# Kernel optimization log

Measured on AMD Instinct MI355X. Metric: run time of the kernel, lower is better.

## Reference

```python
import jax, jax.numpy as jnp
import numpy as np

DIM = 768
H = 12
D = DIM // H            # 64
SCALE = D ** -0.5
M = 64                  # landmarks for pnp heads
PINV_ITERS = 6
PNP_HEADS = 11          # heads 0..10 use Nystrom, head 11 uses softmax


def setup_inputs() -> dict:
    key = jax.random.key(0)
    ks = jax.random.split(key, 5)
    B, N = 4, 4096
    x = jax.random.normal(ks[0], (B, N, DIM), jnp.float32)
    qkv_w = jax.random.normal(ks[1], (3 * DIM, DIM), jnp.float32) * (DIM ** -0.5)
    qkv_b = jax.random.normal(ks[2], (3 * DIM,), jnp.float32) * 0.01
    proj_w = jax.random.normal(ks[3], (DIM, DIM), jnp.float32) * (DIM ** -0.5)
    proj_b = jax.random.normal(ks[4], (DIM,), jnp.float32) * 0.01
    return {"x": x, "qkv_w": qkv_w, "qkv_b": qkv_b, "proj_w": proj_w, "proj_b": proj_b}


def moore_penrose_iter_pinv(x, iters=PINV_ITERS):
    # x: [B, h, M, M]. Original torch code takes torch.max over the whole per-head
    # tensor (incl. batch), so normalize with a per-head scalar over axes (B, M).
    abs_x = jnp.abs(x)
    col_max = abs_x.sum(axis=-1, keepdims=True).max(axis=(0, 2, 3), keepdims=True)
    row_max = abs_x.sum(axis=-2, keepdims=True).max(axis=(0, 2, 3), keepdims=True)
    z = jnp.swapaxes(x, -1, -2) / (col_max * row_max)
    I = jnp.eye(x.shape[-1], dtype=x.dtype)
    for _ in range(iters):
        xz = x @ z
        z = 0.25 * (z @ (13.0 * I - xz @ (15.0 * I - xz @ (7.0 * I - xz))))
    return z


def reference(x, qkv_w, qkv_b, proj_w, proj_b):
    B, N, C = x.shape
    qkv = (x @ qkv_w.T + qkv_b).reshape(B, N, 3, H, D).transpose(2, 0, 3, 1, 4)  # [3,B,H,N,D]
    q, k, v = qkv[0] * SCALE, qkv[1], qkv[2]

    # ---- Nystrom (pnp) heads 0..PNP_HEADS-1, all with the same M -> vectorized ----
    qp, kp, vp = q[:, :PNP_HEADS], k[:, :PNP_HEADS], v[:, :PNP_HEADS]
    idxs = jnp.array([int(i * N / M) for i in range(M)], dtype=jnp.int32)
    q_m = qp[:, :, idxs, :]   # [B,h,M,D] landmark queries
    k_m = kp[:, :, idxs, :]   # [B,h,M,D] landmark keys

    SA = jnp.einsum('bhnd,bhmd->bhnm', qp, k_m)   # [B,h,N,M]
    SC = jnp.einsum('bhmd,bhnd->bhmn', q_m, kp)   # [B,h,M,N]
    SB = jnp.einsum('bhmd,bhld->bhml', q_m, k_m)  # [B,h,M,M]

    eA = jnp.exp(SA - SA.max(axis=-1, keepdims=True))
    sc_max = SC.max(axis=-1, keepdims=True)       # [B,h,M,1]
    eC = jnp.exp(SC - sc_max)
    eB = jnp.exp(jnp.clip(SB - sc_max, -88.0, None))

    v_aug = jnp.concatenate([vp, jnp.ones_like(vp[..., :1])], axis=-1)  # [B,h,N,D+1]
    pi = moore_penrose_iter_pinv(eB)
    prod = (eA @ pi) @ (eC @ v_aug)               # [B,h,N,D+1]
    out_p = prod[..., :-1] / jnp.maximum(prod[..., -1:], 1e-8)

    # ---- fallback softmax head(s) ----
    qs, ks_, vs = q[:, PNP_HEADS:], k[:, PNP_HEADS:], v[:, PNP_HEADS:]
    attn = jax.nn.softmax(jnp.einsum('bhnd,bhmd->bhnm', qs, ks_), axis=-1)
    out_s = attn @ vs

    ctx = jnp.concatenate([out_p, out_s], axis=1).transpose(0, 2, 1, 3).reshape(B, N, C)
    return ctx @ proj_w.T + proj_b
```

## Files before the change

kernel.cpp:

```cpp
#include <hip/hip_runtime.h>


typedef __attribute__((ext_vector_type(8))) short short8;
typedef __attribute__((ext_vector_type(4))) float f32x4;
typedef __attribute__((ext_vector_type(4))) unsigned short ushort4v;

static __device__ __forceinline__ unsigned short f2bf(float f) {
    union { float f; unsigned u; } x; x.f = f;
    unsigned r = x.u + 0x7fffu + ((x.u >> 16) & 1u);
    return (unsigned short)(r >> 16);
}

static __device__ __forceinline__ void bfsplit(float x, unsigned short& h, unsigned short& l) {
    unsigned short hh = f2bf(x);
    union { unsigned u; float f; } t; t.u = (unsigned)hh << 16;
    h = hh;
    l = f2bf(x - t.f);
}

__global__ __launch_bounds__(256) void preconv(
    const float* __restrict__ in, unsigned short* __restrict__ hi,
    unsigned short* __restrict__ lo, int n4)
{
    for (int i = blockIdx.x * 256 + threadIdx.x; i < n4; i += gridDim.x * 256) {
        float4 f = *(const float4*)(in + (size_t)i * 4);
        float vs[4] = {f.x, f.y, f.z, f.w};
        ushort4v h, l;
        #pragma unroll
        for (int j = 0; j < 4; ++j) {
            unsigned short hh, ll;
            bfsplit(vs[j], hh, ll);
            h[j] = hh; l[j] = ll;
        }
        *(ushort4v*)(hi + (size_t)i * 4) = h;
        *(ushort4v*)(lo + (size_t)i * 4) = l;
    }
}

__global__ __launch_bounds__(256, 2) void gemm_qkv_mfma(
    const unsigned short* __restrict__ Xh, const unsigned short* __restrict__ Xl,
    const unsigned short* __restrict__ Wh, const unsigned short* __restrict__ Wl,
    const float* __restrict__ bias,
    float* __restrict__ q, float* __restrict__ k, float* __restrict__ v)
{
    __shared__ unsigned short Ah[4096], Al[4096], Bh[4096], Bl[4096];
    const int tid = threadIdx.x;
    const int bid = blockIdx.x;
    const int swz = (bid & 7) * 288 + (bid >> 3);
    const int brow = (swz / 18) << 7, bcol = (swz % 18) << 7;
    const int ln = tid & 63, wv = tid >> 6;
    const int wr = (wv >> 1) << 6, wc = (wv & 1) << 6;
    const int srow = tid >> 1, sc = (tid & 1) << 1;
    const size_t ag = (size_t)(brow + srow) * 768 + (sc << 3);
    const size_t bg = (size_t)(bcol + srow) * 768 + (sc << 3);
    const int fr = ln & 15, fc = ln >> 4;
    const int i0 = srow * 32 + (((sc + 0) ^ (srow & 3)) << 3);
    const int i1 = srow * 32 + (((sc + 1) ^ (srow & 3)) << 3);

    f32x4 acc[4][4] = {};
    for (int k0 = 0; k0 < 768; k0 += 32) {
        short8 xh0 = *(const short8*)(Xh + ag + k0);
        short8 xh1 = *(const short8*)(Xh + ag + k0 + 8);
        short8 xl0 = *(const short8*)(Xl + ag + k0);
        short8 xl1 = *(const short8*)(Xl + ag + k0 + 8);
        short8 wh0 = *(const short8*)(Wh + bg + k0);
        short8 wh1 = *(const short8*)(Wh + bg + k0 + 8);
        short8 wl0 = *(const short8*)(Wl + bg + k0);
        short8 wl1 = *(const short8*)(Wl + bg + k0 + 8);
        __syncthreads();
        *(short8*)&Ah[i0] = xh0; *(short8*)&Ah[i1] = xh1;
        *(short8*)&Al[i0] = xl0; *(short8*)&Al[i1] = xl1;
        *(short8*)&Bh[i0] = wh0; *(short8*)&Bh[i1] = wh1;
        *(short8*)&Bl[i0] = wl0; *(short8*)&Bl[i1] = wl1;
        __syncthreads();
        short8 ah[4], al[4], bh[4], bl[4];
        #pragma unroll
        for (int i = 0; i < 4; ++i) {
            int ar = wr + (i << 4) + fr;
            int aidx = ar * 32 + ((fc ^ (ar & 3)) << 3);
            ah[i] = *(short8*)&Ah[aidx];
            al[i] = *(short8*)&Al[aidx];
            int br2 = wc + (i << 4) + fr;
            int bidx = br2 * 32 + ((fc ^ (br2 & 3)) << 3);
            bh[i] = *(short8*)&Bh[bidx];
            bl[i] = *(short8*)&Bl[bidx];
        }
        #pragma unroll
        for (int i = 0; i < 4; ++i)
            #pragma unroll
            for (int j = 0; j < 4; ++j) {
                acc[i][j] = __builtin_amdgcn_mfma_f32_16x16x32_bf16(ah[i], bh[j], acc[i][j], 0, 0, 0);
                acc[i][j] = __builtin_amdgcn_mfma_f32_16x16x32_bf16(ah[i], bl[j], acc[i][j], 0, 0, 0);
                acc[i][j] = __builtin_amdgcn_mfma_f32_16x16x32_bf16(al[i], bh[j], acc[i][j], 0, 0, 0);
            }
    }
    const int fg = ln >> 4;
    #pragma unroll
    for (int j = 0; j < 4; ++j) {
        int c = bcol + wc + (j << 4) + fr;
        float bb = bias[c];
        int t = c / 768;
        int rem = c - t * 768;
        int h = rem >> 6, d = rem & 63;
        #pragma unroll
        for (int i = 0; i < 4; ++i)
            #pragma unroll
            for (int r = 0; r < 4; ++r) {
                int row = brow + wr + (i << 4) + (fg << 2) + r;
                int b = row >> 12, n = row & 4095;
                float val = acc[i][j][r] + bb;
                size_t idx = (((size_t)(b * 12 + h) << 12) + n) * 64 + d;
                if (t == 0)      q[idx] = val * 0.125f;
                else if (t == 1) k[idx] = val;
                else             v[idx] = val;
            }
    }
}

__global__ __launch_bounds__(256) void wflash(
    const float* __restrict__ q, const float* __restrict__ k,
    const float* __restrict__ v,
    float* __restrict__ wacc, float* __restrict__ wl, float* __restrict__ wm)
{
    int chunk = blockIdx.x;
    int bh = blockIdx.y;
    int b = bh / 11, h = bh - b * 11;
    size_t base = ((size_t)(b * 12 + h)) << 12;
    const float* qb = q + base * 64;
    const float* kb = k + base * 64;
    const float* vb = v + base * 64;
    __shared__ unsigned short kh[64][72], kl[64][72];
    __shared__ unsigned short vth[64][72], vtl[64][72];
    __shared__ unsigned short ph[4][16][72], pl[4][16][72];
    int tid = threadIdx.x;
    int wv = tid >> 6, ln = tid & 63;
    int rr = tid >> 2, dg = (tid & 3) << 4;
    const int arow = (wv << 4) + (ln & 15);
    const int ak0 = (ln >> 4) << 3;
    const int rg = (ln >> 4) << 2;
    short8 aqh0, aql0, aqh1, aql1;
    {
        const float* qrow = qb + ((size_t)arow << 12);
        #pragma unroll
        for (int j = 0; j < 8; ++j) {
            unsigned short hh, ll;
            bfsplit(qrow[ak0 + j], hh, ll);
            aqh0[j] = (short)hh; aql0[j] = (short)ll;
            bfsplit(qrow[ak0 + 32 + j], hh, ll);
            aqh1[j] = (short)hh; aql1[j] = (short)ll;
        }
    }
    f32x4 o_acc[4] = {};
    float mr[4] = {-1e30f, -1e30f, -1e30f, -1e30f};
    float lr[4] = {};
    for (int t = 0; t < 8; ++t) {
        int n0 = (chunk << 9) + (t << 6);
        __syncthreads();
        {
            const float* krow = kb + (((size_t)(n0 + rr)) << 6) + dg;
            const float* vrow = vb + (((size_t)(n0 + rr)) << 6) + dg;
            #pragma unroll
            for (int i = 0; i < 16; i += 4) {
                float4 f = *(const float4*)(krow + i);
                unsigned short hh, ll;
                bfsplit(f.x, hh, ll); kh[rr][dg+i]   = hh; kl[rr][dg+i]   = ll;
                bfsplit(f.y, hh, ll); kh[rr][dg+i+1] = hh; kl[rr][dg+i+1] = ll;
                bfsplit(f.z, hh, ll); kh[rr][dg+i+2] = hh; kl[rr][dg+i+2] = ll;
                bfsplit(f.w, hh, ll); kh[rr][dg+i+3] = hh; kl[rr][dg+i+3] = ll;
                float4 g2 = *(const float4*)(vrow + i);
                bfsplit(g2.x, hh, ll); vth[dg+i][rr]   = hh; vtl[dg+i][rr]   = ll;
                bfsplit(g2.y, hh, ll); vth[dg+i+1][rr] = hh; vtl[dg+i+1][rr] = ll;
                bfsplit(g2.z, hh, ll); vth[dg+i+2][rr] = hh; vtl[dg+i+2][rr] = ll;
                bfsplit(g2.w, hh, ll); vth[dg+i+3][rr] = hh; vtl[dg+i+3][rr] = ll;
            }
        }
        __syncthreads();
        f32x4 s_acc[4];
        #pragma unroll
        for (int jb = 0; jb < 4; ++jb) {
            f32x4 z = {};
            const int brow2 = (jb << 4) + (ln & 15);
            short8 bh0 = *(short8*)&kh[brow2][ak0];
            short8 bh1 = *(short8*)&kh[brow2][ak0 + 32];
            short8 bl0 = *(short8*)&kl[brow2][ak0];
            short8 bl1 = *(short8*)&kl[brow2][ak0 + 32];
            z = __builtin_amdgcn_mfma_f32_16x16x32_bf16(aqh0, bh0, z, 0, 0, 0);
            z = __builtin_amdgcn_mfma_f32_16x16x32_bf16(aqh0, bl0, z, 0, 0, 0);
            z = __builtin_amdgcn_mfma_f32_16x16x32_bf16(aql0, bh0, z, 0, 0, 0);
            z = __builtin_amdgcn_mfma_f32_16x16x32_bf16(aqh1, bh1, z, 0, 0, 0);
            z = __builtin_amdgcn_mfma_f32_16x16x32_bf16(aqh1, bl1, z, 0, 0, 0);
            z = __builtin_amdgcn_mfma_f32_16x16x32_bf16(aql1, bh1, z, 0, 0, 0);
            s_acc[jb] = z;
        }
        float mx[4];
        #pragma unroll
        for (int r = 0; r < 4; ++r)
            mx[r] = fmaxf(fmaxf(s_acc[0][r], s_acc[1][r]),
                          fmaxf(s_acc[2][r], s_acc[3][r]));
        #pragma unroll
        for (int off = 1; off < 16; off <<= 1)
            #pragma unroll
            for (int r = 0; r < 4; ++r)
                mx[r] = fmaxf(mx[r], __shfl_xor(mx[r], off, 64));
        float fac[4];
        #pragma unroll
        for (int r = 0; r < 4; ++r) {
            float mn = fmaxf(mr[r], mx[r]);
            fac[r] = expf(mr[r] - mn);
            mr[r] = mn;
        }
        float rs[4] = {};
        #pragma unroll
        for (int jb = 0; jb < 4; ++jb)
            #pragma unroll
            for (int r = 0; r < 4; ++r) {
                float p = expf(s_acc[jb][r] - mr[r]);
                rs[r] += p;
                unsigned short hh, ll;
                bfsplit(p, hh, ll);
                ph[wv][rg + r][(jb << 4) + (ln & 15)] = hh;
                pl[wv][rg + r][(jb << 4) + (ln & 15)] = ll;
            }
        #pragma unroll
        for (int off = 1; off < 16; off <<= 1)
            #pragma unroll
            for (int r = 0; r < 4; ++r)
                rs[r] += __shfl_xor(rs[r], off, 64);
        #pragma unroll
        for (int r = 0; r < 4; ++r) lr[r] = lr[r] * fac[r] + rs[r];
        #pragma unroll
        for (int jb = 0; jb < 4; ++jb)
            #pragma unroll
            for (int r = 0; r < 4; ++r)
                o_acc[jb][r] *= fac[r];
        short8 pah0 = *(short8*)&ph[wv][ln & 15][ak0];
        short8 pah1 = *(short8*)&ph[wv][ln & 15][ak0 + 32];
        short8 pal0 = *(short8*)&pl[wv][ln & 15][ak0];
        short8 pal1 = *(short8*)&pl[wv][ln & 15][ak0 + 32];
        #pragma unroll
        for (int jb = 0; jb < 4; ++jb) {
            const int brow2 = (jb << 4) + (ln & 15);
            short8 bvh0 = *(short8*)&vth[brow2][ak0];
            short8 bvh1 = *(short8*)&vth[brow2][ak0 + 32];
            short8 bvl0 = *(short8*)&vtl[brow2][ak0];
            short8 bvl1 = *(short8*)&vtl[brow2][ak0 + 32];
            f32x4 o = o_acc[jb];
            o = __builtin_amdgcn_mfma_f32_16x16x32_bf16(pah0, bvh0, o, 0, 0, 0);
            o = __builtin_amdgcn_mfma_f32_16x16x32_bf16(pah0, bvl0, o, 0, 0, 0);
            o = __builtin_amdgcn_mfma_f32_16x16x32_bf16(pal0, bvh0, o, 0, 0, 0);
            o = __builtin_amdgcn_mfma_f32_16x16x32_bf16(pah1, bvh1, o, 0, 0, 0);
            o = __builtin_amdgcn_mfma_f32_16x16x32_bf16(pah1, bvl1, o, 0, 0, 0);
            o = __builtin_amdgcn_mfma_f32_16x16x32_bf16(pal1, bvh1, o, 0, 0, 0);
            o_acc[jb] = o;
        }
    }
    int cidx = (bh << 3) + chunk;
    #pragma unroll
    for (int jb = 0; jb < 4; ++jb)
        #pragma unroll
        for (int r = 0; r < 4; ++r) {
            int row = (wv << 4) + rg + r, col = (jb << 4) + (ln & 15);
            wacc[((size_t)cidx << 12) + ((size_t)row << 6) + col] = o_acc[jb][r];
        }
    if ((ln & 15) == 0)
        #pragma unroll
        for (int r = 0; r < 4; ++r) {
            int row = (wv << 4) + rg + r;
            wl[cidx * 64 + row] = lr[r];
            wm[cidx * 64 + row] = mr[r];
        }
}

__global__ __launch_bounds__(256) void wmerge(
    const float* __restrict__ wacc, const float* __restrict__ wl,
    const float* __restrict__ wm,
    float* __restrict__ Wb, float* __restrict__ scm)
{
    int bh = blockIdx.x;
    int tid = threadIdx.x;
    __shared__ float fcs[8][64];
    if (tid < 64) {
        float mx = -1e30f;
        #pragma unroll
        for (int c = 0; c < 8; ++c)
            mx = fmaxf(mx, wm[((bh << 3) + c) * 64 + tid]);
        scm[(bh << 6) + tid] = mx;
        #pragma unroll
        for (int c = 0; c < 8; ++c)
            fcs[c][tid] = expf(wm[((bh << 3) + c) * 64 + tid] - mx);
    }
    __syncthreads();
    for (int e = tid; e < 4096; e += 256) {
        int m = e >> 6, j = e & 63;
        float s = 0.f;
        #pragma unroll
        for (int c = 0; c < 8; ++c)
            s += fcs[c][m] * wacc[((size_t)((bh << 3) + c) << 12) + e];
        Wb[(size_t)bh * 4160 + m * 65 + j] = s;
    }
    if (tid < 64) {
        float s = 0.f;
        #pragma unroll
        for (int c = 0; c < 8; ++c)
            s += fcs[c][tid] * wl[((bh << 3) + c) * 64 + tid];
        Wb[(size_t)bh * 4160 + tid * 65 + 64] = s;
    }
}

__global__ __launch_bounds__(256) void eb_kernel(
    const float* __restrict__ q, const float* __restrict__ k,
    const float* __restrict__ scm, float* __restrict__ eB)
{
    int bh = blockIdx.x;
    int b = bh / 11, h = bh - b * 11;
    size_t base = ((size_t)(b * 12 + h)) << 12;
    const float* qb = q + base * 64;
    const float* kb = k + base * 64;
    __shared__ float qm[64][65], km[64][65];
    int tid = threadIdx.x;
    for (int e = tid; e < 4096; e += 256) {
        int mm = e >> 6, d = e & 63;
        qm[mm][d] = qb[((size_t)mm << 12) + d];
        km[mm][d] = kb[((size_t)mm << 12) + d];
    }
    __syncthreads();
    int m = tid >> 2, l0 = tid & 3;
    float smax = scm[(bh << 6) + m];
    for (int l = l0; l < 64; l += 4) {
        float s = 0.f;
        #pragma unroll
        for (int d = 0; d < 64; ++d) s += qm[m][d] * km[l][d];
        eB[((size_t)bh << 12) + (m << 6) + l] = expf(fmaxf(s - smax, -88.f));
    }
}

__global__ __launch_bounds__(256) void norms_kernel(
    const float* __restrict__ eB, float* __restrict__ denom)
{
    int h = blockIdx.x;
    int tid = threadIdx.x;
    int b = tid >> 6, idx = tid & 63;
    int bh = b * 11 + h;
    const float* E = eB + ((size_t)bh << 12);
    float rs = 0.f, cs = 0.f;
    #pragma unroll 4
    for (int l = 0; l < 64; ++l) rs += E[(idx << 6) + l];
    #pragma unroll 4
    for (int m = 0; m < 64; ++m) cs += E[(m << 6) + idx];
    __shared__ float r1[256], r2[256];
    r1[tid] = rs; r2[tid] = cs;
    __syncthreads();
    for (int s = 128; s > 0; s >>= 1) {
        if (tid < s) {
            r1[tid] = fmaxf(r1[tid], r1[tid + s]);
            r2[tid] = fmaxf(r2[tid], r2[tid + s]);
        }
        __syncthreads();
    }
    if (tid == 0) denom[h] = r1[0] * r2[0];
}

__device__ __forceinline__ void mm64x3(
    const unsigned short (&Ahi)[64][72], const unsigned short (&Alo)[64][72],
    const unsigned short (&BThi)[64][72], const unsigned short (&BTlo)[64][72],
    int wr, int wc, int fr, int fk, f32x4 (&acc)[2][2])
{
    #pragma unroll
    for (int ks = 0; ks < 2; ++ks) {
        const int kb = (ks << 5) + fk;
        short8 ah[2], al[2], bh[2], bl[2];
        #pragma unroll
        for (int i = 0; i < 2; ++i) {
            ah[i] = *(const short8*)&Ahi[wr + (i << 4) + fr][kb];
            al[i] = *(const short8*)&Alo[wr + (i << 4) + fr][kb];
            bh[i] = *(const short8*)&BThi[wc + (i << 4) + fr][kb];
            bl[i] = *(const short8*)&BTlo[wc + (i << 4) + fr][kb];
// ... 101 lines not shown
                for (int r = 0; r < 4; ++r) {
                    int row = wr + (i << 4) + rg + r, col = wc + (j << 4) + fr;
                    zn[i][j][r] = 0.25f * (13.f * Zf[row][col] - a4[i][j][r]);
                }
        __syncthreads();
        #pragma unroll
        for (int i = 0; i < 2; ++i)
            #pragma unroll
            for (int j = 0; j < 2; ++j)
                #pragma unroll
                for (int r = 0; r < 4; ++r) {
                    int row = wr + (i << 4) + rg + r, col = wc + (j << 4) + fr;
                    float val = zn[i][j][r];
                    Zf[row][col] = val;
                    unsigned short hh, ll;
                    bfsplit(val, hh, ll);
                    Zh[row][col] = hh;  Zl[row][col] = ll;
                    ZTh[col][row] = hh; ZTl[col][row] = ll;
                }
        __syncthreads();
    }
    for (int e = tid; e < 4096; e += 256)
        pi_[((size_t)bh << 12) + e] = Zf[e >> 6][e & 63];
}

__global__ __launch_bounds__(256) void pw_kernel(
    const float* __restrict__ pi_, const float* __restrict__ Wb,
    float* __restrict__ Tb)
{
    int bh = blockIdx.x;
    __shared__ float P[64][65];
    __shared__ float Wl[64][66];
    int tid = threadIdx.x;
    for (int e = tid; e < 4096; e += 256)
        P[e >> 6][e & 63] = pi_[((size_t)bh << 12) + e];
    for (int e = tid; e < 64 * 65; e += 256) {
        int l = e / 65, j = e - l * 65;
        Wl[l][j] = Wb[(size_t)bh * 4160 + e];
    }
    __syncthreads();
    int m = tid & 63, g = tid >> 6;
    #pragma unroll
    for (int t = 0; t < 17; ++t) {
        int j = g + (t << 2);
        if (j > 64) break;
        float s = 0.f;
        #pragma unroll
        for (int l = 0; l < 64; ++l) s += P[m][l] * Wl[l][j];
        Tb[(size_t)((bh << 6) + m) * 65 + j] = s;
    }
}

__global__ __launch_bounds__(256) void outp_kernel(
    const float* __restrict__ q, const float* __restrict__ k,
    const float* __restrict__ Tb, unsigned short* __restrict__ ctxh)
{
    int bh = blockIdx.y;
    int b = bh / 11, h = bh - b * 11;
    int n0 = blockIdx.x << 6;
    size_t base = ((size_t)(b * 12 + h)) << 12;
    const float* qb = q + base * 64;
    const float* kb = k + base * 64;
    __shared__ unsigned short kmh[64][72], kml[64][72];
    __shared__ unsigned short tth[64][72], ttl[64][72];
    __shared__ unsigned short ph[4][16][72], pl[4][16][72];
    __shared__ float t64[64];
    int tid = threadIdx.x;
    int wv = tid >> 6, ln = tid & 63;
    int rr = tid >> 2, dg = (tid & 3) << 4;
    const int arow = (wv << 4) + (ln & 15);
    const int ak0 = (ln >> 4) << 3;
    const int rg = (ln >> 4) << 2;
    {
        const float* krow = kb + ((size_t)rr << 12) + dg;
        #pragma unroll
        for (int i = 0; i < 16; i += 4) {
            float4 f = *(const float4*)(krow + i);
            unsigned short hh, ll;
            bfsplit(f.x, hh, ll); kmh[rr][dg+i]   = hh; kml[rr][dg+i]   = ll;
            bfsplit(f.y, hh, ll); kmh[rr][dg+i+1] = hh; kml[rr][dg+i+1] = ll;
            bfsplit(f.z, hh, ll); kmh[rr][dg+i+2] = hh; kml[rr][dg+i+2] = ll;
            bfsplit(f.w, hh, ll); kmh[rr][dg+i+3] = hh; kml[rr][dg+i+3] = ll;
        }
    }
    for (int e = tid; e < 4096; e += 256) {
        int m = e >> 6, j = e & 63;
        float tv = Tb[(size_t)((bh << 6) + m) * 65 + j];
        unsigned short hh, ll;
        bfsplit(tv, hh, ll);
        tth[j][m] = hh; ttl[j][m] = ll;
    }
    if (tid < 64) t64[tid] = Tb[(size_t)((bh << 6) + tid) * 65 + 64];
    short8 aqh0, aql0, aqh1, aql1;
    {
        const float* qrow = qb + (((size_t)(n0 + arow)) << 6);
        #pragma unroll
        for (int j = 0; j < 8; ++j) {
            unsigned short hh, ll;
            bfsplit(qrow[ak0 + j], hh, ll);
            aqh0[j] = (short)hh; aql0[j] = (short)ll;
            bfsplit(qrow[ak0 + 32 + j], hh, ll);
            aqh1[j] = (short)hh; aql1[j] = (short)ll;
        }
    }
    __syncthreads();
    f32x4 s_acc[4];
    #pragma unroll
    for (int jb = 0; jb < 4; ++jb) {
        f32x4 z = {};
        const int brow2 = (jb << 4) + (ln & 15);
        short8 bh0 = *(short8*)&kmh[brow2][ak0];
        short8 bh1 = *(short8*)&kmh[brow2][ak0 + 32];
        short8 bl0 = *(short8*)&kml[brow2][ak0];
        short8 bl1 = *(short8*)&kml[brow2][ak0 + 32];
        z = __builtin_amdgcn_mfma_f32_16x16x32_bf16(aqh0, bh0, z, 0, 0, 0);
        z = __builtin_amdgcn_mfma_f32_16x16x32_bf16(aqh0, bl0, z, 0, 0, 0);
        z = __builtin_amdgcn_mfma_f32_16x16x32_bf16(aql0, bh0, z, 0, 0, 0);
        z = __builtin_amdgcn_mfma_f32_16x16x32_bf16(aqh1, bh1, z, 0, 0, 0);
        z = __builtin_amdgcn_mfma_f32_16x16x32_bf16(aqh1, bl1, z, 0, 0, 0);
        z = __builtin_amdgcn_mfma_f32_16x16x32_bf16(aql1, bh1, z, 0, 0, 0);
        s_acc[jb] = z;
    }
    float mx[4];
    #pragma unroll
    for (int r = 0; r < 4; ++r)
        mx[r] = fmaxf(fmaxf(s_acc[0][r], s_acc[1][r]),
                      fmaxf(s_acc[2][r], s_acc[3][r]));
    #pragma unroll
    for (int off = 1; off < 16; off <<= 1)
        #pragma unroll
        for (int r = 0; r < 4; ++r)
            mx[r] = fmaxf(mx[r], __shfl_xor(mx[r], off, 64));
    float den[4] = {};
    #pragma unroll
    for (int jb = 0; jb < 4; ++jb) {
        float tj = t64[(jb << 4) + (ln & 15)];
        #pragma unroll
        for (int r = 0; r < 4; ++r) {
            float p = expf(s_acc[jb][r] - mx[r]);
            den[r] += p * tj;
            unsigned short hh, ll;
            bfsplit(p, hh, ll);
            ph[wv][rg + r][(jb << 4) + (ln & 15)] = hh;
            pl[wv][rg + r][(jb << 4) + (ln & 15)] = ll;
        }
    }
    #pragma unroll
    for (int off = 1; off < 16; off <<= 1)
        #pragma unroll
        for (int r = 0; r < 4; ++r)
            den[r] += __shfl_xor(den[r], off, 64);
    short8 pah0 = *(short8*)&ph[wv][ln & 15][ak0];
    short8 pah1 = *(short8*)&ph[wv][ln & 15][ak0 + 32];
    short8 pal0 = *(short8*)&pl[wv][ln & 15][ak0];
    short8 pal1 = *(short8*)&pl[wv][ln & 15][ak0 + 32];
    f32x4 o_acc[4] = {};
    #pragma unroll
    for (int jb = 0; jb < 4; ++jb) {
        const int brow2 = (jb << 4) + (ln & 15);
        short8 bth0 = *(short8*)&tth[brow2][ak0];
        short8 bth1 = *(short8*)&tth[brow2][ak0 + 32];
        short8 btl0 = *(short8*)&ttl[brow2][ak0];
        short8 btl1 = *(short8*)&ttl[brow2][ak0 + 32];
        f32x4 o = o_acc[jb];
        o = __builtin_amdgcn_mfma_f32_16x16x32_bf16(pah0, bth0, o, 0, 0, 0);
        o = __builtin_amdgcn_mfma_f32_16x16x32_bf16(pah0, btl0, o, 0, 0, 0);
        o = __builtin_amdgcn_mfma_f32_16x16x32_bf16(pal0, bth0, o, 0, 0, 0);
        o = __builtin_amdgcn_mfma_f32_16x16x32_bf16(pah1, bth1, o, 0, 0, 0);
        o = __builtin_amdgcn_mfma_f32_16x16x32_bf16(pah1, btl1, o, 0, 0, 0);
        o = __builtin_amdgcn_mfma_f32_16x16x32_bf16(pal1, bth1, o, 0, 0, 0);
        o_acc[jb] = o;
    }
    float inv[4];
    #pragma unroll
    for (int r = 0; r < 4; ++r) inv[r] = 1.0f / fmaxf(den[r], 1e-8f);
    #pragma unroll
    for (int jb = 0; jb < 4; ++jb)
        #pragma unroll
        for (int r = 0; r < 4; ++r) {
            int row = n0 + (wv << 4) + rg + r;
            int col = (jb << 4) + (ln & 15);
            ctxh[((size_t)b * 4096 + row) * 768 + h * 64 + col] =
                f2bf(o_acc[jb][r] * inv[r]);
        }
}

__global__ __launch_bounds__(256) void flash_part(
    const float* __restrict__ q, const float* __restrict__ k,
    const float* __restrict__ v,
    float* __restrict__ pacc, float* __restrict__ pm, float* __restrict__ pl)
{
    int bx = blockIdx.x, cy = blockIdx.y, b = blockIdx.z;
    int n0 = bx << 6;
    size_t base = ((size_t)(b * 12 + 11)) << 12;
    const float* qb = q + base * 64;
    const float* kb = k + base * 64;
    const float* vb = v + base * 64;
    __shared__ unsigned short qs[64][72];
    __shared__ unsigned short ks[64][72];
    __shared__ unsigned short vts[64][72];
    __shared__ unsigned short ps[4][16][72];
    int tid = threadIdx.x;
    int wv = tid >> 6, ln = tid & 63;
    int rr = tid >> 2, dg = (tid & 3) << 4;
    for (int e = tid * 4; e < 4096; e += 1024) {
        int r2 = e >> 6, d = e & 63;
        float4 f = *(const float4*)(qb + (((size_t)(n0 + r2)) << 6) + d);
        qs[r2][d] = f2bf(f.x); qs[r2][d+1] = f2bf(f.y);
        qs[r2][d+2] = f2bf(f.z); qs[r2][d+3] = f2bf(f.w);
    }
    __syncthreads();
    const int arow = (wv << 4) + (ln & 15);
    const int ak0 = (ln >> 4) << 3;
    const int rg = (ln >> 4) << 2;
    short8 aq0 = *(short8*)&qs[arow][ak0];
    short8 aq1 = *(short8*)&qs[arow][ak0 + 32];
    f32x4 o_acc[4] = {};
    float mr[4] = {-1e30f, -1e30f, -1e30f, -1e30f};
    float lr[4] = {};
    for (int t = 0; t < 16; ++t) {
        int m0 = (cy << 10) + (t << 6);
        __syncthreads();
        {
            const float* krow = kb + (((size_t)(m0 + rr)) << 6) + dg;
            const float* vrow = vb + (((size_t)(m0 + rr)) << 6) + dg;
            #pragma unroll
            for (int i = 0; i < 16; i += 4) {
                float4 f = *(const float4*)(krow + i);
                ks[rr][dg+i] = f2bf(f.x); ks[rr][dg+i+1] = f2bf(f.y);
                ks[rr][dg+i+2] = f2bf(f.z); ks[rr][dg+i+3] = f2bf(f.w);
                float4 g2 = *(const float4*)(vrow + i);
                vts[dg+i][rr] = f2bf(g2.x); vts[dg+i+1][rr] = f2bf(g2.y);
                vts[dg+i+2][rr] = f2bf(g2.z); vts[dg+i+3][rr] = f2bf(g2.w);
            }
        }
        __syncthreads();
        f32x4 s_acc[4];
        #pragma unroll
        for (int jb = 0; jb < 4; ++jb) {
            f32x4 z = {};
            short8 bk0 = *(short8*)&ks[(jb << 4) + (ln & 15)][ak0];
            short8 bk1 = *(short8*)&ks[(jb << 4) + (ln & 15)][ak0 + 32];
            z = __builtin_amdgcn_mfma_f32_16x16x32_bf16(aq0, bk0, z, 0, 0, 0);
            z = __builtin_amdgcn_mfma_f32_16x16x32_bf16(aq1, bk1, z, 0, 0, 0);
            s_acc[jb] = z;
        }
        float mx[4];
        #pragma unroll
        for (int r = 0; r < 4; ++r)
            mx[r] = fmaxf(fmaxf(s_acc[0][r], s_acc[1][r]),
                          fmaxf(s_acc[2][r], s_acc[3][r]));
        #pragma unroll
        for (int off = 1; off < 16; off <<= 1)
            #pragma unroll
            for (int r = 0; r < 4; ++r)
                mx[r] = fmaxf(mx[r], __shfl_xor(mx[r], off, 64));
        float fac[4];
        #pragma unroll
        for (int r = 0; r < 4; ++r) {
            float mn = fmaxf(mr[r], mx[r]);
            fac[r] = expf(mr[r] - mn);
            mr[r] = mn;
        }
        float rs[4] = {};
        #pragma unroll
        for (int jb = 0; jb < 4; ++jb)
            #pragma unroll
            for (int r = 0; r < 4; ++r) {
                float p = expf(s_acc[jb][r] - mr[r]);
                rs[r] += p;
                ps[wv][rg + r][(jb << 4) + (ln & 15)] = f2bf(p);
            }
        #pragma unroll
        for (int off = 1; off < 16; off <<= 1)
            #pragma unroll
            for (int r = 0; r < 4; ++r)
                rs[r] += __shfl_xor(rs[r], off, 64);
        #pragma unroll
        for (int r = 0; r < 4; ++r) lr[r] = lr[r] * fac[r] + rs[r];
        #pragma unroll
        for (int jb = 0; jb < 4; ++jb)
            #pragma unroll
            for (int r = 0; r < 4; ++r)
                o_acc[jb][r] *= fac[r];
        short8 pa0 = *(short8*)&ps[wv][ln & 15][ak0];
        short8 pa1 = *(short8*)&ps[wv][ln & 15][ak0 + 32];
        #pragma unroll
        for (int jb = 0; jb < 4; ++jb) {
            short8 bv0 = *(short8*)&vts[(jb << 4) + (ln & 15)][ak0];
            short8 bv1 = *(short8*)&vts[(jb << 4) + (ln & 15)][ak0 + 32];
            f32x4 z = o_acc[jb];
            z = __builtin_amdgcn_mfma_f32_16x16x32_bf16(pa0, bv0, z, 0, 0, 0);
            z = __builtin_amdgcn_mfma_f32_16x16x32_bf16(pa1, bv1, z, 0, 0, 0);
            o_acc[jb] = z;
        }
    }
    int slot = (b * 4 + cy) * 64 + bx;
    #pragma unroll
    for (int jb = 0; jb < 4; ++jb)
        #pragma unroll
        for (int r = 0; r < 4; ++r) {
            int row = (wv << 4) + rg + r, col = (jb << 4) + (ln & 15);
            pacc[(size_t)slot * 4096 + (size_t)row * 64 + col] = o_acc[jb][r];
        }
    if ((ln & 15) == 0)
        #pragma unroll
        for (int r = 0; r < 4; ++r) {
            int row = (wv << 4) + rg + r;
            pm[(size_t)slot * 64 + row] = mr[r];
            pl[(size_t)slot * 64 + row] = lr[r];
        }
}

__global__ __launch_bounds__(256) void flash_merge(
    const float* __restrict__ pacc, const float* __restrict__ pm,
    const float* __restrict__ pl, unsigned short* __restrict__ ctxh)
{
    int bx = blockIdx.x, b = blockIdx.y;
    int tid = threadIdx.x, r = tid & 63, g = tid >> 6;
    float mc[4], mt = -1e30f;
    #pragma unroll
    for (int c = 0; c < 4; ++c) {
        mc[c] = pm[(size_t)((b * 4 + c) * 64 + bx) * 64 + r];
        mt = fmaxf(mt, mc[c]);
    }
    float fac[4], lt = 0.f;
    #pragma unroll
    for (int c = 0; c < 4; ++c) {
        fac[c] = expf(mc[c] - mt);
        lt += fac[c] * pl[(size_t)((b * 4 + c) * 64 + bx) * 64 + r];
// ... 28 lines not shown
    const int i0 = srow * 32 + (((sc + 0) ^ (srow & 3)) << 3);
    const int i1 = srow * 32 + (((sc + 1) ^ (srow & 3)) << 3);

    f32x4 acc[4][4] = {};
    for (int k0 = 0; k0 < 768; k0 += 32) {
        short8 xh0 = *(const short8*)(Xh + ag + k0);
        short8 xh1 = *(const short8*)(Xh + ag + k0 + 8);
        short8 wh0 = *(const short8*)(Wh + bg + k0);
        short8 wh1 = *(const short8*)(Wh + bg + k0 + 8);
        __syncthreads();
        *(short8*)&Ah[i0] = xh0; *(short8*)&Ah[i1] = xh1;
        *(short8*)&Bh[i0] = wh0; *(short8*)&Bh[i1] = wh1;
        __syncthreads();
        short8 ah[4], bh[4];
        #pragma unroll
        for (int i = 0; i < 4; ++i) {
            int ar = wr + (i << 4) + fr;
            ah[i] = *(short8*)&Ah[ar * 32 + ((fc ^ (ar & 3)) << 3)];
            int br2 = wc + (i << 4) + fr;
            bh[i] = *(short8*)&Bh[br2 * 32 + ((fc ^ (br2 & 3)) << 3)];
        }
        #pragma unroll
        for (int i = 0; i < 4; ++i)
            #pragma unroll
            for (int j = 0; j < 4; ++j)
                acc[i][j] = __builtin_amdgcn_mfma_f32_16x16x32_bf16(ah[i], bh[j], acc[i][j], 0, 0, 0);
    }
    const int fg = ln >> 4;
    #pragma unroll
    for (int j = 0; j < 4; ++j) {
        int c = bcol + wc + (j << 4) + fr;
        float bb = bias[c];
        #pragma unroll
        for (int i = 0; i < 4; ++i)
            #pragma unroll
            for (int r = 0; r < 4; ++r) {
                int row = brow + wr + (i << 4) + (fg << 2) + r;
                out[(size_t)row * 768 + c] = acc[i][j][r] + bb;
            }
    }
}

extern "C" void kernel_launch(void* const* d_in, const int* in_sizes, int n_in,
                              void* d_out, int out_size, void* d_ws, size_t ws_size,
                              hipStream_t stream)
{
    const float* x      = (const float*)d_in[0];
    const float* qkv_w  = (const float*)d_in[1];
    const float* qkv_b  = (const float*)d_in[2];
    const float* proj_w = (const float*)d_in[3];
    const float* proj_b = (const float*)d_in[4];
    float* out = (float*)d_out;

    float* ws  = (float*)d_ws;
    const size_t QKV = (size_t)4 * 12 * 4096 * 64;
    float* q    = ws;
    float* k    = q + QKV;
    float* v    = k + QKV;
    unsigned short* ctxh = (unsigned short*)(v + QKV);
    float* scm  = (float*)(ctxh + QKV);
    float* eB   = scm + 4096;
    float* den  = eB + 44 * 4096;
    float* pi_  = den + 64;
    float* Wb   = pi_ + 44 * 4096;
    float* Tb   = Wb + 44 * 4160;
    unsigned short* Whi  = (unsigned short*)(Tb + 44 * 4160);
    unsigned short* Wlo  = Whi + (size_t)2304 * 768;
    unsigned short* Pwhi = Wlo + (size_t)2304 * 768;
    unsigned short* Pwlo = Pwhi + (size_t)768 * 768;

    unsigned short* Xhi = (unsigned short*)out;
    unsigned short* Xlo = Xhi + QKV;
    float* wacc = out;
    float* wl   = wacc + 1441792;
    float* wm   = wl + 22528;
    float* fpacc = out;
    float* fpm   = fpacc + 4194304;
    float* fpl   = fpm + 65536;

    preconv<<<2048, 256, 0, stream>>>(x, Xhi, Xlo, 3145728);
    preconv<<<1024, 256, 0, stream>>>(qkv_w, Whi, Wlo, 442368);
    preconv<<<512, 256, 0, stream>>>(proj_w, Pwhi, Pwlo, 147456);
    gemm_qkv_mfma<<<2304, 256, 0, stream>>>(Xhi, Xlo, Whi, Wlo, qkv_b, q, k, v);
    wflash<<<dim3(8, 44), 256, 0, stream>>>(q, k, v, wacc, wl, wm);
    wmerge<<<44, 256, 0, stream>>>(wacc, wl, wm, Wb, scm);
    eb_kernel<<<44, 256, 0, stream>>>(q, k, scm, eB);
    norms_kernel<<<11, 256, 0, stream>>>(eB, den);
    pinv_kernel<<<44, 256, 0, stream>>>(eB, den, pi_);
    pw_kernel<<<44, 256, 0, stream>>>(pi_, Wb, Tb);
    outp_kernel<<<dim3(64, 44), 256, 0, stream>>>(q, k, Tb, ctxh);
    flash_part<<<dim3(64, 4, 4), 256, 0, stream>>>(q, k, v, fpacc, fpm, fpl);
    flash_merge<<<dim3(64, 4), 256, 0, stream>>>(fpacc, fpm, fpl, ctxh);
    gemm_proj_mfma<<<768, 256, 0, stream>>>(ctxh, Pwhi, proj_b, out);
}
```

Measured before the change: 495.6 us.

## Emit bf16 hi/lo split Q/K and bf16 V from QKV GEMM epilogue

The QKV GEMM epilogue now writes Q and K as bf16 hi/lo pairs and V as single bf16, in place of fp32. Downstream attention kernels load these pre-split operands directly and skip the repeated per-tile bfsplit conversions. The V projection drops the two low-order MFMA correction terms, and the P·V products in wflash use only bf16 V. This cuts GEMM MFMA work for a third of the columns, reduces global traffic, and removes redundant conversion arithmetic, at the cost of lower V precision in the Nystrom path.

```diff
diff --git a/kernel.cpp b/kernel.cpp
--- a/kernel.cpp
+++ b/kernel.cpp
@@ -9,6 +9,10 @@
     union { float f; unsigned u; } x; x.f = f;
     unsigned r = x.u + 0x7fffu + ((x.u >> 16) & 1u);
     return (unsigned short)(r >> 16);
+}
+
+static __device__ __forceinline__ float b2f(unsigned short u) {
+    union { unsigned u; float f; } t; t.u = (unsigned)u << 16; return t.f;
 }
 
 static __device__ __forceinline__ void bfsplit(float x, unsigned short& h, unsigned short& l) {
@@ -41,13 +45,16 @@
     const unsigned short* __restrict__ Xh, const unsigned short* __restrict__ Xl,
     const unsigned short* __restrict__ Wh, const unsigned short* __restrict__ Wl,
     const float* __restrict__ bias,
-    float* __restrict__ q, float* __restrict__ k, float* __restrict__ v)
+    unsigned short* __restrict__ qh, unsigned short* __restrict__ ql,
+    unsigned short* __restrict__ kh, unsigned short* __restrict__ kl,
+    unsigned short* __restrict__ vh)
 {
     __shared__ unsigned short Ah[4096], Al[4096], Bh[4096], Bl[4096];
     const int tid = threadIdx.x;
     const int bid = blockIdx.x;
     const int swz = (bid & 7) * 288 + (bid >> 3);
     const int brow = (swz / 18) << 7, bcol = (swz % 18) << 7;
+    const bool isv = (bcol >= 1536);
     const int ln = tid & 63, wv = tid >> 6;
     const int wr = (wv >> 1) << 6, wc = (wv & 1) << 6;
     const int srow = tid >> 1, sc = (tid & 1) << 1;
@@ -61,17 +68,22 @@
     for (int k0 = 0; k0 < 768; k0 += 32) {
         short8 xh0 = *(const short8*)(Xh + ag + k0);
         short8 xh1 = *(const short8*)(Xh + ag + k0 + 8);
-        short8 xl0 = *(const short8*)(Xl + ag + k0);
-        short8 xl1 = *(const short8*)(Xl + ag + k0 + 8);
         short8 wh0 = *(const short8*)(Wh + bg + k0);
         short8 wh1 = *(const short8*)(Wh + bg + k0 + 8);
-        short8 wl0 = *(const short8*)(Wl + bg + k0);
-        short8 wl1 = *(const short8*)(Wl + bg + k0 + 8);
+        short8 xl0, xl1, wl0, wl1;
+        if (!isv) {
+            xl0 = *(const short8*)(Xl + ag + k0);
+            xl1 = *(const short8*)(Xl + ag + k0 + 8);
+            wl0 = *(const short8*)(Wl + bg + k0);
+            wl1 = *(const short8*)(Wl + bg + k0 + 8);
+        }
         __syncthreads();
         *(short8*)&Ah[i0] = xh0; *(short8*)&Ah[i1] = xh1;
-        *(short8*)&Al[i0] = xl0; *(short8*)&Al[i1] = xl1;
         *(short8*)&Bh[i0] = wh0; *(short8*)&Bh[i1] = wh1;
-        *(short8*)&Bl[i0] = wl0; *(short8*)&Bl[i1] = wl1;
+        if (!isv) {
+            *(short8*)&Al[i0] = xl0; *(short8*)&Al[i1] = xl1;
+            *(short8*)&Bl[i0] = wl0; *(short8*)&Bl[i1] = wl1;
+        }
         __syncthreads();
         short8 ah[4], al[4], bh[4], bl[4];
         #pragma unroll
@@ -79,19 +91,23 @@
             int ar = wr + (i << 4) + fr;
             int aidx = ar * 32 + ((fc ^ (ar & 3)) << 3);
             ah[i] = *(short8*)&Ah[aidx];
-            al[i] = *(short8*)&Al[aidx];
             int br2 = wc + (i << 4) + fr;
             int bidx = br2 * 32 + ((fc ^ (br2 & 3)) << 3);
             bh[i] = *(short8*)&Bh[bidx];
-            bl[i] = *(short8*)&Bl[bidx];
+            if (!isv) {
+                al[i] = *(short8*)&Al[aidx];
+                bl[i] = *(short8*)&Bl[bidx];
+            }
         }
         #pragma unroll
         for (int i = 0; i < 4; ++i)
             #pragma unroll
             for (int j = 0; j < 4; ++j) {
                 acc[i][j] = __builtin_amdgcn_mfma_f32_16x16x32_bf16(ah[i], bh[j], acc[i][j], 0, 0, 0);
-                acc[i][j] = __builtin_amdgcn_mfma_f32_16x16x32_bf16(ah[i], bl[j], acc[i][j], 0, 0, 0);
-                acc[i][j] = __builtin_amdgcn_mfma_f32_16x16x32_bf16(al[i], bh[j], acc[i][j], 0, 0, 0);
+                if (!isv) {
+                    acc[i][j] = __builtin_amdgcn_mfma_f32_16x16x32_bf16(ah[i], bl[j], acc[i][j], 0, 0, 0);
+                    acc[i][j] = __builtin_amdgcn_mfma_f32_16x16x32_bf16(al[i], bh[j], acc[i][j], 0, 0, 0);
+                }
             }
     }
     const int fg = ln >> 4;
@@ -110,27 +126,32 @@
                 int b = row >> 12, n = row & 4095;
                 float val = acc[i][j][r] + bb;
                 size_t idx = (((size_t)(b * 12 + h) << 12) + n) * 64 + d;
-                if (t == 0)      q[idx] = val * 0.125f;
-                else if (t == 1) k[idx] = val;
-                else             v[idx] = val;
+                unsigned short hh, ll;
+                if (t == 0) {
+                    bfsplit(val * 0.125f, hh, ll);
+                    qh[idx] = hh; ql[idx] = ll;
+                } else if (t == 1) {
+                    bfsplit(val, hh, ll);
+                    kh[idx] = hh; kl[idx] = ll;
+                } else {
+                    vh[idx] = f2bf(val);
+                }
             }
     }
 }
 
 __global__ __launch_bounds__(256) void wflash(
-    const float* __restrict__ q, const float* __restrict__ k,
-    const float* __restrict__ v,
+    const unsigned short* __restrict__ qh, const unsigned short* __restrict__ ql,
+    const unsigned short* __restrict__ khg, const unsigned short* __restrict__ klg,
+    const unsigned short* __restrict__ vhg,
     float* __restrict__ wacc, float* __restrict__ wl, float* __restrict__ wm)
 {
     int chunk = blockIdx.x;
     int bh = blockIdx.y;
     int b = bh / 11, h = bh - b * 11;
     size_t base = ((size_t)(b * 12 + h)) << 12;
-    const float* qb = q + base * 64;
-    const float* kb = k + base * 64;
-    const float* vb = v + base * 64;
-    __shared__ unsigned short kh[64][72], kl[64][72];
-    __shared__ unsigned short vth[64][72], vtl[64][72];
+    __shared__ unsigned short kh_s[64][72], kl_s[64][72];
+    __shared__ unsigned short vth[64][72];
     __shared__ unsigned short ph[4][16][72], pl[4][16][72];
     int tid = threadIdx.x;
     int wv = tid >> 6, ln = tid & 63;
@@ -140,15 +161,11 @@
     const int rg = (ln >> 4) << 2;
     short8 aqh0, aql0, aqh1, aql1;
     {
-        const float* qrow = qb + ((size_t)arow << 12);
-        #pragma unroll
-        for (int j = 0; j < 8; ++j) {
-            unsigned short hh, ll;
-            bfsplit(qrow[ak0 + j], hh, ll);
-            aqh0[j] = (short)hh; aql0[j] = (short)ll;
-            bfsplit(qrow[ak0 + 32 + j], hh, ll);
-            aqh1[j] = (short)hh; aql1[j] = (short)ll;
-        }
+        size_t off = ((base + ((size_t)arow << 6)) << 6) + ak0;
+        aqh0 = *(const short8*)(qh + off);
+        aqh1 = *(const short8*)(qh + off + 32);
+        aql0 = *(const short8*)(ql + off);
+        aql1 = *(const short8*)(ql + off + 32);
     }
     f32x4 o_acc[4] = {};
     float mr[4] = {-1e30f, -1e30f, -1e30f, -1e30f};
@@ -157,21 +174,17 @@
         int n0 = (chunk << 9) + (t << 6);
         __syncthreads();
         {
-            const float* krow = kb + (((size_t)(n0 + rr)) << 6) + dg;
-            const float* vrow = vb + (((size_t)(n0 + rr)) << 6) + dg;
-            #pragma unroll
-            for (int i = 0; i < 16; i += 4) {
-                float4 f = *(const float4*)(krow + i);
-                unsigned short hh, ll;
-                bfsplit(f.x, hh, ll); kh[rr][dg+i]   = hh; kl[rr][dg+i]   = ll;
-                bfsplit(f.y, hh, ll); kh[rr][dg+i+1] = hh; kl[rr][dg+i+1] = ll;
-                bfsplit(f.z, hh, ll); kh[rr][dg+i+2] = hh; kl[rr][dg+i+2] = ll;
-                bfsplit(f.w, hh, ll); kh[rr][dg+i+3] = hh; kl[rr][dg+i+3] = ll;
-                float4 g2 = *(const float4*)(vrow + i);
-                bfsplit(g2.x, hh, ll); vth[dg+i][rr]   = hh; vtl[dg+i][rr]   = ll;
-                bfsplit(g2.y, hh, ll); vth[dg+i+1][rr] = hh; vtl[dg+i+1][rr] = ll;
-                bfsplit(g2.z, hh, ll); vth[dg+i+2][rr] = hh; vtl[dg+i+2][rr] = ll;
-                bfsplit(g2.w, hh, ll); vth[dg+i+3][rr] = hh; vtl[dg+i+3][rr] = ll;
+            size_t off = ((base + n0 + rr) << 6) + dg;
+            *(short8*)&kh_s[rr][dg]     = *(const short8*)(khg + off);
+            *(short8*)&kh_s[rr][dg + 8] = *(const short8*)(khg + off + 8);
+            *(short8*)&kl_s[rr][dg]     = *(const short8*)(klg + off);
+            *(short8*)&kl_s[rr][dg + 8] = *(const short8*)(klg + off + 8);
+            short8 v0 = *(const short8*)(vhg + off);
+            short8 v1 = *(const short8*)(vhg + off + 8);
+            #pragma unroll
+            for (int i = 0; i < 8; ++i) {
+                vth[dg + i][rr]     = (unsigned short)v0[i];
+                vth[dg + 8 + i][rr] = (unsigned short)v1[i];
             }
         }
         __syncthreads();
@@ -180,10 +193,10 @@
         for (int jb = 0; jb < 4; ++jb) {
             f32x4 z = {};
             const int brow2 = (jb << 4) + (ln & 15);
-            short8 bh0 = *(short8*)&kh[brow2][ak0];
-            short8 bh1 = *(short8*)&kh[brow2][ak0 + 32];
-            short8 bl0 = *(short8*)&kl[brow2][ak0];
-            short8 bl1 = *(short8*)&kl[brow2][ak0 + 32];
+            short8 bh0 = *(short8*)&kh_s[brow2][ak0];
+            short8 bh1 = *(short8*)&kh_s[brow2][ak0 + 32];
+            short8 bl0 = *(short8*)&kl_s[brow2][ak0];
+            short8 bl1 = *(short8*)&kl_s[brow2][ak0 + 32];
             z = __builtin_amdgcn_mfma_f32_16x16x32_bf16(aqh0, bh0, z, 0, 0, 0);
             z = __builtin_amdgcn_mfma_f32_16x16x32_bf16(aqh0, bl0, z, 0, 0, 0);
             z = __builtin_amdgcn_mfma_f32_16x16x32_bf16(aql0, bh0, z, 0, 0, 0);
@@ -198,10 +211,10 @@
             mx[r] = fmaxf(fmaxf(s_acc[0][r], s_acc[1][r]),
                           fmaxf(s_acc[2][r], s_acc[3][r]));
         #pragma unroll
-        for (int off = 1; off < 16; off <<= 1)
+        for (int off2 = 1; off2 < 16; off2 <<= 1)
             #pragma unroll
             for (int r = 0; r < 4; ++r)
-                mx[r] = fmaxf(mx[r], __shfl_xor(mx[r], off, 64));
+                mx[r] = fmaxf(mx[r], __shfl_xor(mx[r], off2, 64));
         float fac[4];
         #pragma unroll
         for (int r = 0; r < 4; ++r) {
@@ -222,10 +235,10 @@
                 pl[wv][rg + r][(jb << 4) + (ln & 15)] = ll;
             }
         #pragma unroll
-        for (int off = 1; off < 16; off <<= 1)
+        for (int off2 = 1; off2 < 16; off2 <<= 1)
             #pragma unroll
             for (int r = 0; r < 4; ++r)
-                rs[r] += __shfl_xor(rs[r], off, 64);
+                rs[r] += __shfl_xor(rs[r], off2, 64);
         #pragma unroll
         for (int r = 0; r < 4; ++r) lr[r] = lr[r] * fac[r] + rs[r];
         #pragma unroll
@@ -240,17 +253,13 @@
         #pragma unroll
         for (int jb = 0; jb < 4; ++jb) {
             const int brow2 = (jb << 4) + (ln & 15);
-            short8 bvh0 = *(short8*)&vth[brow2][ak0];
-            short8 bvh1 = *(short8*)&vth[brow2][ak0 + 32];
-            short8 bvl0 = *(short8*)&vtl[brow2][ak0];
-            short8 bvl1 = *(short8*)&vtl[brow2][ak0 + 32];
+            short8 bv0 = *(short8*)&vth[brow2][ak0];
+            short8 bv1 = *(short8*)&vth[brow2][ak0 + 32];
             f32x4 o = o_acc[jb];
-            o = __builtin_amdgcn_mfma_f32_16x16x32_bf16(pah0, bvh0, o, 0, 0, 0);
-            o = __builtin_amdgcn_mfma_f32_16x16x32_bf16(pah0, bvl0, o, 0, 0, 0);
-            o = __builtin_amdgcn_mfma_f32_16x16x32_bf16(pal0, bvh0, o, 0, 0, 0);
-            o = __builtin_amdgcn_mfma_f32_16x16x32_bf16(pah1, bvh1, o, 0, 0, 0);
-            o = __builtin_amdgcn_mfma_f32_16x16x32_bf16(pah1, bvl1, o, 0, 0, 0);
-            o = __builtin_amdgcn_mfma_f32_16x16x32_bf16(pal1, bvh1, o, 0, 0, 0);
+            o = __builtin_amdgcn_mfma_f32_16x16x32_bf16(pah0, bv0, o, 0, 0, 0);
+            o = __builtin_amdgcn_mfma_f32_16x16x32_bf16(pal0, bv0, o, 0, 0, 0);
+            o = __builtin_amdgcn_mfma_f32_16x16x32_bf16(pah1, bv1, o, 0, 0, 0);
+            o = __builtin_amdgcn_mfma_f32_16x16x32_bf16(pal1, bv1, o, 0, 0, 0);
             o_acc[jb] = o;
         }
     }
@@ -308,20 +317,20 @@
 }
 
 __global__ __launch_bounds__(256) void eb_kernel(
-    const float* __restrict__ q, const float* __restrict__ k,
+    const unsigned short* __restrict__ qh, const unsigned short* __restrict__ ql,
+    const unsigned short* __restrict__ kh, const unsigned short* __restrict__ kl,
     const float* __restrict__ scm, float* __restrict__ eB)
 {
     int bh = blockIdx.x;
     int b = bh / 11, h = bh - b * 11;
     size_t base = ((size_t)(b * 12 + h)) << 12;
-    const float* qb = q + base * 64;
-    const float* kb = k + base * 64;
     __shared__ float qm[64][65], km[64][65];
     int tid = threadIdx.x;
     for (int e = tid; e < 4096; e += 256) {
         int mm = e >> 6, d = e & 63;
-        qm[mm][d] = qb[((size_t)mm << 12) + d];
-        km[mm][d] = kb[((size_t)mm << 12) + d];
+        size_t off = ((base + ((size_t)mm << 6)) << 6) + d;
+        qm[mm][d] = b2f(qh[off]) + b2f(ql[off]);
+        km[mm][d] = b2f(kh[off]) + b2f(kl[off]);
     }
     __syncthreads();
     int m = tid >> 2, l0 = tid & 3;
@@ -529,15 +538,14 @@
 }
 
 __global__ __launch_bounds__(256) void outp_kernel(
-    const float* __restrict__ q, const float* __restrict__ k,
+    const unsigned short* __restrict__ qh, const unsigned short* __restrict__ ql,
+    const unsigned short* __restrict__ khg, const unsigned short* __restrict__ klg,
     const float* __restrict__ Tb, unsigned short* __restrict__ ctxh)
 {
     int bh = blockIdx.y;
     int b = bh / 11, h = bh - b * 11;
     int n0 = blockIdx.x << 6;
     size_t base = ((size_t)(b * 12 + h)) << 12;
-    const float* qb = q + base * 64;
-    const float* kb = k + base * 64;
     __shared__ unsigned short kmh[64][72], kml[64][72];
     __shared__ unsigned short tth[64][72], ttl[64][72];
     __shared__ unsigned short ph[4][16][72], pl[4][16][72];
@@ -549,16 +557,11 @@
     const int ak0 = (ln >> 4) << 3;
     const int rg = (ln >> 4) << 2;
     {
-        const float* krow = kb + ((size_t)rr << 12) + dg;
-        #pragma unroll
-        for (int i = 0; i < 16; i += 4) {
-            float4 f = *(const float4*)(krow + i);
-            unsigned short hh, ll;
-            bfsplit(f.x, hh, ll); kmh[rr][dg+i]   = hh; kml[rr][dg+i]   = ll;
-            bfsplit(f.y, hh, ll); kmh[rr][dg+i+1] = hh; kml[rr][dg+i+1] = ll;
-            bfsplit(f.z, hh, ll); kmh[rr][dg+i+2] = hh; kml[rr][dg+i+2] = ll;
-            bfsplit(f.w, hh, ll); kmh[rr][dg+i+3] = hh; kml[rr][dg+i+3] = ll;
-        }
+        size_t off = ((base + ((size_t)rr << 6)) << 6) + dg;
+        *(short8*)&kmh[rr][dg]     = *(const short8*)(khg + off);
+        *(short8*)&kmh[rr][dg + 8] = *(const short8*)(khg + off + 8);
+        *(short8*)&kml[rr][dg]     = *(const short8*)(klg + off);
+        *(short8*)&kml[rr][dg + 8] = *(const short8*)(klg + off + 8);
     }
     for (int e = tid; e < 4096; e += 256) {
         int m = e >> 6, j = e & 63;
@@ -570,15 +573,11 @@
     if (tid < 64) t64[tid] = Tb[(size_t)((bh << 6) + tid) * 65 + 64];
     short8 aqh0, aql0, aqh1, aql1;
     {
-        const float* qrow = qb + (((size_t)(n0 + arow)) << 6);
-        #pragma unroll
-        for (int j = 0; j < 8; ++j) {
-            unsigned short hh, ll;
-            bfsplit(qrow[ak0 + j], hh, ll);
-            aqh0[j] = (short)hh; aql0[j] = (short)ll;
-            bfsplit(qrow[ak0 + 32 + j], hh, ll);
-            aqh1[j] = (short)hh; aql1[j] = (short)ll;
-        }
+        size_t off = ((base + n0 + arow) << 6) + ak0;
+        aqh0 = *(const short8*)(qh + off);
+        aqh1 = *(const short8*)(qh + off + 32);
+        aql0 = *(const short8*)(ql + off);
+        aql1 = *(const short8*)(ql + off + 32);
     }
     __syncthreads();
     f32x4 s_acc[4];
@@ -604,10 +603,10 @@
         mx[r] = fmaxf(fmaxf(s_acc[0][r], s_acc[1][r]),
                       fmaxf(s_acc[2][r], s_acc[3][r]));
     #pragma unroll
-    for (int off = 1; off < 16; off <<= 1)
+    for (int off2 = 1; off2 < 16; off2 <<= 1)
         #pragma unroll
         for (int r = 0; r < 4; ++r)
-            mx[r] = fmaxf(mx[r], __shfl_xor(mx[r], off, 64));
+            mx[r] = fmaxf(mx[r], __shfl_xor(mx[r], off2, 64));
     float den[4] = {};
     #pragma unroll
     for (int jb = 0; jb < 4; ++jb) {
@@ -623,10 +622,10 @@
         }
     }
     #pragma unroll
-    for (int off = 1; off < 16; off <<= 1)
+    for (int off2 = 1; off2 < 16; off2 <<= 1)
         #pragma unroll
         for (int r = 0; r < 4; ++r)
-            den[r] += __shfl_xor(den[r], off, 64);
+            den[r] += __shfl_xor(den[r], off2, 64);
     short8 pah0 = *(short8*)&ph[wv][ln & 15][ak0];
     short8 pah1 = *(short8*)&ph[wv][ln & 15][ak0 + 32];
     short8 pal0 = *(short8*)&pl[wv][ln & 15][ak0];
@@ -663,16 +662,13 @@
 }
 
 __global__ __launch_bounds__(256) void flash_part(
-    const float* __restrict__ q, const float* __restrict__ k,
-    const float* __restrict__ v,
+    const unsigned short* __restrict__ qhg, const unsigned short* __restrict__ khg,
+    const unsigned short* __restrict__ vhg,
     float* __restrict__ pacc, float* __restrict__ pm, float* __restrict__ pl)
 {
     int bx = blockIdx.x, cy = blockIdx.y, b = blockIdx.z;
     int n0 = bx << 6;
     size_t base = ((size_t)(b * 12 + 11)) << 12;
-    const float* qb = q + base * 64;
-    const float* kb = k + base * 64;
-    const float* vb = v + base * 64;
     __shared__ unsigned short qs[64][72];
     __shared__ unsigned short ks[64][72];
     __shared__ unsigned short vts[64][72];
@@ -680,11 +676,10 @@
     int tid = threadIdx.x;
     int wv = tid >> 6, ln = tid & 63;
     int rr = tid >> 2, dg = (tid & 3) << 4;
-    for (int e = tid * 4; e < 4096; e += 1024) {
-        int r2 = e >> 6, d = e & 63;
-        float4 f = *(const float4*)(qb + (((size_t)(n0 + r2)) << 6) + d);
-        qs[r2][d] = f2bf(f.x); qs[r2][d+1] = f2bf(f.y);
-        qs[r2][d+2] = f2bf(f.z); qs[r2][d+3] = f2bf(f.w);
+    {
+        size_t off = ((base + n0 + rr) << 6) + dg;
+        *(short8*)&qs[rr][dg]     = *(const short8*)(qhg + off);
+        *(short8*)&qs[rr][dg + 8] = *(const short8*)(qhg + off + 8);
     }
     __syncthreads();
     const int arow = (wv << 4) + (ln & 15);
@@ -699,16 +694,15 @@
         int m0 = (cy << 10) + (t << 6);
         __syncthreads();
         {
-            const float* krow = kb + (((size_t)(m0 + rr)) << 6) + dg;
-            const float* vrow = vb + (((size_t)(m0 + rr)) << 6) + dg;
-            #pragma unroll
-            for (int i = 0; i < 16; i += 4) {
-                float4 f = *(const float4*)(krow + i);
-                ks[rr][dg+i] = f2bf(f.x); ks[rr][dg+i+1] = f2bf(f.y);
-                ks[rr][dg+i+2] = f2bf(f.z); ks[rr][dg+i+3] = f2bf(f.w);
-                float4 g2 = *(const float4*)(vrow + i);
-                vts[dg+i][rr] = f2bf(g2.x); vts[dg+i+1][rr] = f2bf(g2.y);
-                vts[dg+i+2][rr] = f2bf(g2.z); vts[dg+i+3][rr] = f2bf(g2.w);
+            size_t off = ((base + m0 + rr) << 6) + dg;
+            *(short8*)&ks[rr][dg]     = *(const short8*)(khg + off);
+            *(short8*)&ks[rr][dg + 8] = *(const short8*)(khg + off + 8);
+            short8 v0 = *(const short8*)(vhg + off);
+            short8 v1 = *(const short8*)(vhg + off + 8);
+            #pragma unroll
+            for (int i = 0; i < 8; ++i) {
+                vts[dg + i][rr]     = (unsigned short)v0[i];
+                vts[dg + 8 + i][rr] = (unsigned short)v1[i];
             }
         }
         __syncthreads();
@@ -728,10 +722,10 @@
             mx[r] = fmaxf(fmaxf(s_acc[0][r], s_acc[1][r]),
                           fmaxf(s_acc[2][r], s_acc[3][r]));
         #pragma unroll
-        for (int off = 1; off < 16; off <<= 1)
+        for (int off2 = 1; off2 < 16; off2 <<= 1)
             #pragma unroll
             for (int r = 0; r < 4; ++r)
-                mx[r] = fmaxf(mx[r], __shfl_xor(mx[r], off, 64));
+                mx[r] = fmaxf(mx[r], __shfl_xor(mx[r], off2, 64));
         float fac[4];
         #pragma unroll
         for (int r = 0; r < 4; ++r) {
@@ -749,10 +743,10 @@
                 ps[wv][rg + r][(jb << 4) + (ln & 15)] = f2bf(p);
             }
         #pragma unroll
-        for (int off = 1; off < 16; off <<= 1)
+        for (int off2 = 1; off2 < 16; off2 <<= 1)
             #pragma unroll
             for (int r = 0; r < 4; ++r)
-                rs[r] += __shfl_xor(rs[r], off, 64);
+                rs[r] += __shfl_xor(rs[r], off2, 64);
         #pragma unroll
         for (int r = 0; r < 4; ++r) lr[r] = lr[r] * fac[r] + rs[r];
         #pragma unroll
@@ -887,12 +881,13 @@
     const float* proj_b = (const float*)d_in[4];
     float* out = (float*)d_out;
 
-    float* ws  = (float*)d_ws;
     const size_t QKV = (size_t)4 * 12 * 4096 * 64;
-    float* q    = ws;
-    float* k    = q + QKV;
-    float* v    = k + QKV;
-    unsigned short* ctxh = (unsigned short*)(v + QKV);
+    unsigned short* qh = (unsigned short*)d_ws;
+    unsigned short* ql = qh + QKV;
+    unsigned short* kh = ql + QKV;
+    unsigned short* kl = kh + QKV;
+    unsigned short* vh = kl + QKV;
+    unsigned short* ctxh = vh + QKV;
     float* scm  = (float*)(ctxh + QKV);
     float* eB   = scm + 4096;
     float* den  = eB + 44 * 4096;
@@ -916,15 +911,16 @@
     preconv<<<2048, 256, 0, stream>>>(x, Xhi, Xlo, 3145728);
     preconv<<<1024, 256, 0, stream>>>(qkv_w, Whi, Wlo, 442368);
     preconv<<<512, 256, 0, stream>>>(proj_w, Pwhi, Pwlo, 147456);
-    gemm_qkv_mfma<<<2304, 256, 0, stream>>>(Xhi, Xlo, Whi, Wlo, qkv_b, q, k, v);
-    wflash<<<dim3(8, 44), 256, 0, stream>>>(q, k, v, wacc, wl, wm);
+    gemm_qkv_mfma<<<2304, 256, 0, stream>>>(Xhi, Xlo, Whi, Wlo, qkv_b,
+                                            qh, ql, kh, kl, vh);
+    wflash<<<dim3(8, 44), 256, 0, stream>>>(qh, ql, kh, kl, vh, wacc, wl, wm);
     wmerge<<<44, 256, 0, stream>>>(wacc, wl, wm, Wb, scm);
-    eb_kernel<<<44, 256, 0, stream>>>(q, k, scm, eB);
+    eb_kernel<<<44, 256, 0, stream>>>(qh, ql, kh, kl, scm, eB);
     norms_kernel<<<11, 256, 0, stream>>>(eB, den);
     pinv_kernel<<<44, 256, 0, stream>>>(eB, den, pi_);
     pw_kernel<<<44, 256, 0, stream>>>(pi_, Wb, Tb);
-    outp_kernel<<<dim3(64, 44), 256, 0, stream>>>(q, k, Tb, ctxh);
-    flash_part<<<dim3(64, 4, 4), 256, 0, stream>>>(q, k, v, fpacc, fpm, fpl);
+    outp_kernel<<<dim3(64, 44), 256, 0, stream>>>(qh, ql, kh, kl, Tb, ctxh);
+    flash_part<<<dim3(64, 4, 4), 256, 0, stream>>>(qh, kh, vh, fpacc, fpm, fpl);
     flash_merge<<<dim3(64, 4), 256, 0, stream>>>(fpacc, fpm, fpl, ctxh);
     gemm_proj_mfma<<<768, 256, 0, stream>>>(ctxh, Pwhi, proj_b, out);
 }
```

After: 480.4 us. -3.1%, faster.
